# Kernel tuning notes

Measured on AMD Instinct MI355X. Metric: run time of the kernel, lower is better.

## Reference

```python
import jax, jax.numpy as jnp
import numpy as np

CELL = 7
NBOX = 2
NCLS = 20


def _grid_indicies(s):
    # matches torch _generate_grid: channel 0 = column index (x), channel 1 = row index (y)
    gx = jnp.broadcast_to(jnp.arange(s, dtype=jnp.float32)[None, :], (s, s))
    gy = jnp.broadcast_to(jnp.arange(s, dtype=jnp.float32)[:, None], (s, s))
    return jnp.stack([gx, gy])[None]  # (1, 2, s, s)


def setup_inputs() -> dict:
    key = jax.random.key(0)
    x = jax.random.uniform(key, (16384, NCLS + 5 * NBOX, CELL, CELL), dtype=jnp.float32)
    return {"x": x}


def reference(x):
    B, _, S, _ = x.shape
    gi = _grid_indicies(S).astype(x.dtype)          # (1,2,S,S)
    cls = x[:, -NCLS:, :, :]                        # (B,C,S,S)
    boxes_l, scores_l, idxs_l = [], [], []
    for b in range(NBOX):
        det = x[:, b * 5:(b + 1) * 5]               # (B,5,S,S)
        weighted = cls * det[:, 4:5]                # class probs * objectness
        flat = weighted.reshape(B, NCLS, S * S)     # (B,C,S*S)
        idxs_l.append(flat.argmax(axis=1).astype(x.dtype))
        scores_l.append(flat.max(axis=1))
        center = (det[:, :2] + gi) / S              # relative box center
        half = det[:, 2:4] / 2
        xymin = (center - half).reshape(B, 2, S * S).transpose(0, 2, 1)
        xymax = (center + half).reshape(B, 2, S * S).transpose(0, 2, 1)
        boxes_l.append(jnp.concatenate([xymin, xymax], axis=2))  # (B,S*S,4)
    boxes = jnp.concatenate(boxes_l, axis=1)        # (B, 2*S*S, 4)
    scores = jnp.concatenate(scores_l, axis=1)      # (B, 2*S*S)
    idxs = jnp.concatenate(idxs_l, axis=1)          # (B, 2*S*S) float, as in torch code
    return boxes, scores, idxs
```

## Files before the change

kernel.cpp:

```cpp
#include <hip/hip_runtime.h>

#define NCLS 20

__global__ __launch_bounds__(256) void yolo_kernel(const float* __restrict__ x,
                                                   float* __restrict__ boxes,
                                                   float* __restrict__ scores,
                                                   float* __restrict__ idxs,
                                                   int B) {
    int t = blockIdx.x * blockDim.x + threadIdx.x;
    int total = B * 49;
    if (t >= total) return;
    int batch = t / 49;
    int cell = t - batch * 49;
    int row = cell / 7;
    int col = cell - row * 7;

    const float* xb = x + (size_t)batch * 30 * 49 + cell;

    float cls[NCLS];
    #pragma unroll
    for (int i = 0; i < NCLS; ++i) cls[i] = xb[(10 + i) * 49];

    float gx = (float)col;
    float gy = (float)row;

    #pragma unroll
    for (int b = 0; b < 2; ++b) {
        float d0   = xb[(b * 5 + 0) * 49];
        float d1   = xb[(b * 5 + 1) * 49];
        float d2   = xb[(b * 5 + 2) * 49];
        float d3   = xb[(b * 5 + 3) * 49];
        float conf = xb[(b * 5 + 4) * 49];

        float best = cls[0] * conf;
        int bi = 0;
        #pragma unroll
        for (int i = 1; i < NCLS; ++i) {
            float w = cls[i] * conf;
            if (w > best) { best = w; bi = i; }
        }

        float cxv = (d0 + gx) / 7.0f;
        float cyv = (d1 + gy) / 7.0f;
        float hx = d2 * 0.5f;
        float hy = d3 * 0.5f;

        int orow = b * 49 + cell;
        size_t obase = (size_t)batch * 98 + orow;
        float4 bx = make_float4(cxv - hx, cyv - hy, cxv + hx, cyv + hy);
        *reinterpret_cast<float4*>(boxes + obase * 4) = bx;
        scores[obase] = best;
        idxs[obase]   = (float)bi;
    }
}

extern "C" void kernel_launch(void* const* d_in, const int* in_sizes, int n_in,
                              void* d_out, int out_size, void* d_ws, size_t ws_size,
                              hipStream_t stream) {
    const float* x = (const float*)d_in[0];
    int B = in_sizes[0] / (30 * 49);

    float* out    = (float*)d_out;
    float* boxes  = out;
    float* scores = out + (size_t)B * 98 * 4;
    float* idxs   = scores + (size_t)B * 98;

    int total = B * 49;
    int block = 256;
    int grid = (total + block - 1) / block;
    hipLaunchKernelGGL(yolo_kernel, dim3(grid), dim3(block), 0, stream,
                       x, boxes, scores, idxs, B);
}
```

Measured before the change: 27.21 us.

## Stage per-block batch tiles in LDS with vectorized float4 loads

Each block now copies eight whole batch items (1470 floats each) into shared memory with contiguous float4 loads, then computes cells from LDS. This replaces strided 4-byte global loads across channels with fully coalesced wide loads. It drops bounds checks and assumes B is a multiple of 8. About 47 KB of LDS per block lowers occupancy, and with no overlap between load and compute that may limit latency hiding.

```diff
diff --git a/kernel.cpp b/kernel.cpp
--- a/kernel.cpp
+++ b/kernel.cpp
@@ -1,56 +1,67 @@
 #include <hip/hip_runtime.h>
 
 #define NCLS 20
+#define BPB 8
+#define FPB 1470
+#define LDS_FLOATS (BPB * FPB)
+#define LDS_VEC4   (LDS_FLOATS / 4)
 
 __global__ __launch_bounds__(256) void yolo_kernel(const float* __restrict__ x,
                                                    float* __restrict__ boxes,
                                                    float* __restrict__ scores,
-                                                   float* __restrict__ idxs,
-                                                   int B) {
-    int t = blockIdx.x * blockDim.x + threadIdx.x;
-    int total = B * 49;
-    if (t >= total) return;
-    int batch = t / 49;
-    int cell = t - batch * 49;
-    int row = cell / 7;
-    int col = cell - row * 7;
+                                                   float* __restrict__ idxs) {
+    __shared__ float lds[LDS_FLOATS];
+    const int blk = blockIdx.x;
+    const int tid = threadIdx.x;
 
-    const float* xb = x + (size_t)batch * 30 * 49 + cell;
+    const float4* src = reinterpret_cast<const float4*>(x + (size_t)blk * LDS_FLOATS);
+    float4* dst = reinterpret_cast<float4*>(lds);
+    for (int i = tid; i < LDS_VEC4; i += 256) dst[i] = src[i];
 
-    float cls[NCLS];
-    #pragma unroll
-    for (int i = 0; i < NCLS; ++i) cls[i] = xb[(10 + i) * 49];
+    __syncthreads();
 
-    float gx = (float)col;
-    float gy = (float)row;
+    for (int c = tid; c < BPB * 49; c += 256) {
+        int bl = c / 49;
+        int cell = c - bl * 49;
+        int row = cell / 7;
+        int col = cell - row * 7;
+        const float* xb = lds + bl * FPB + cell;
 
-    #pragma unroll
-    for (int b = 0; b < 2; ++b) {
-        float d0   = xb[(b * 5 + 0) * 49];
-        float d1   = xb[(b * 5 + 1) * 49];
-        float d2   = xb[(b * 5 + 2) * 49];
-        float d3   = xb[(b * 5 + 3) * 49];
-        float conf = xb[(b * 5 + 4) * 49];
+        float cls[NCLS];
+        #pragma unroll
+        for (int i = 0; i < NCLS; ++i) cls[i] = xb[(10 + i) * 49];
 
-        float best = cls[0] * conf;
-        int bi = 0;
+        float gx = (float)col;
+        float gy = (float)row;
+        int batch = blk * BPB + bl;
+
         #pragma unroll
-        for (int i = 1; i < NCLS; ++i) {
-            float w = cls[i] * conf;
-            if (w > best) { best = w; bi = i; }
+        for (int b = 0; b < 2; ++b) {
+            float d0   = xb[(b * 5 + 0) * 49];
+            float d1   = xb[(b * 5 + 1) * 49];
+            float d2   = xb[(b * 5 + 2) * 49];
+            float d3   = xb[(b * 5 + 3) * 49];
+            float conf = xb[(b * 5 + 4) * 49];
+
+            float best = cls[0] * conf;
+            int bi = 0;
+            #pragma unroll
+            for (int i = 1; i < NCLS; ++i) {
+                float w = cls[i] * conf;
+                if (w > best) { best = w; bi = i; }
+            }
+
+            float cxv = (d0 + gx) / 7.0f;
+            float cyv = (d1 + gy) / 7.0f;
+            float hx = d2 * 0.5f;
+            float hy = d3 * 0.5f;
+
+            size_t obase = (size_t)batch * 98 + b * 49 + cell;
+            *reinterpret_cast<float4*>(boxes + obase * 4) =
+                make_float4(cxv - hx, cyv - hy, cxv + hx, cyv + hy);
+            scores[obase] = best;
+            idxs[obase]   = (float)bi;
         }
-
-        float cxv = (d0 + gx) / 7.0f;
-        float cyv = (d1 + gy) / 7.0f;
-        float hx = d2 * 0.5f;
-        float hy = d3 * 0.5f;
-
-        int orow = b * 49 + cell;
-        size_t obase = (size_t)batch * 98 + orow;
-        float4 bx = make_float4(cxv - hx, cyv - hy, cxv + hx, cyv + hy);
-        *reinterpret_cast<float4*>(boxes + obase * 4) = bx;
-        scores[obase] = best;
-        idxs[obase]   = (float)bi;
     }
 }
 
@@ -58,16 +69,14 @@
                               void* d_out, int out_size, void* d_ws, size_t ws_size,
                               hipStream_t stream) {
     const float* x = (const float*)d_in[0];
-    int B = in_sizes[0] / (30 * 49);
+    int B = in_sizes[0] / FPB;
 
     float* out    = (float*)d_out;
     float* boxes  = out;
     float* scores = out + (size_t)B * 98 * 4;
     float* idxs   = scores + (size_t)B * 98;
 
-    int total = B * 49;
-    int block = 256;
-    int grid = (total + block - 1) / block;
-    hipLaunchKernelGGL(yolo_kernel, dim3(grid), dim3(block), 0, stream,
-                       x, boxes, scores, idxs, B);
+    int grid = B / BPB;
+    hipLaunchKernelGGL(yolo_kernel, dim3(grid), dim3(256), 0, stream,
+                       x, boxes, scores, idxs);
 }
```

Measured after the change: 29.40 us. 8.1% more time.
